# Optimization experiments

Measured on AMD Instinct MI355X. Metric: run time of the kernel, lower is better.

Reference implementation:

```python
import jax, jax.numpy as jnp
import numpy as np

B, N, D = 8, 1024, 512
H = 8
DH = D // H
EPS_DIST = 1e-8
EPS_LN = 1e-5


def _layer_norm(x, gamma, beta):
    mu = jnp.mean(x, axis=-1, keepdims=True)
    var = jnp.mean((x - mu) ** 2, axis=-1, keepdims=True)
    return (x - mu) * jax.lax.rsqrt(var + EPS_LN) * gamma + beta


def setup_inputs() -> dict:
    key = jax.random.key(0)
    ks = jax.random.split(key, 6)
    scale = 1.0 / np.sqrt(D)
    inp = {
        "x": jax.random.normal(ks[0], (B, N, D), dtype=jnp.float32),
        "Wq": jax.random.normal(ks[1], (D, D), dtype=jnp.float32) * scale,
        "Wk": jax.random.normal(ks[2], (D, D), dtype=jnp.float32) * scale,
        "Wv": jax.random.normal(ks[3], (D, D), dtype=jnp.float32) * scale,
        "Wo": jax.random.normal(ks[4], (D, D), dtype=jnp.float32) * scale,
        "bq": jnp.zeros((D,), jnp.float32),
        "bk": jnp.zeros((D,), jnp.float32),
        "bv": jnp.zeros((D,), jnp.float32),
        "bo": jnp.zeros((D,), jnp.float32),
        "ln1_g": jnp.ones((D,), jnp.float32),
        "ln1_b": jnp.zeros((D,), jnp.float32),
        "ln2_g": jnp.ones((D,), jnp.float32),
        "ln2_b": jnp.zeros((D,), jnp.float32),
    }
    return inp


def reference(x, Wq, bq, Wk, bk, Wv, bv, Wo, bo, ln1_g, ln1_b, ln2_g, ln2_b):
    residual = x
    h = _layer_norm(x, ln1_g, ln1_b)  # pre-norm

    def heads(t):
        # [B,N,D] -> [B,H,N,DH]
        return t.reshape(B, N, H, DH).transpose(0, 2, 1, 3)

    q = heads(h @ Wq + bq)
    k = heads(h @ Wk + bk)
    v = heads(h @ Wv + bv)

    # Euclidean pairwise distance via ||q||^2 + ||k||^2 - 2 q.k expansion
    q_sq = jnp.sum(q * q, axis=-1)[..., :, None]      # [B,H,N,1]
    k_sq = jnp.sum(k * k, axis=-1)[..., None, :]      # [B,H,1,N]
    qk = jnp.einsum("bhnd,bhmd->bhnm", q, k)          # [B,H,N,N]
    d2 = jnp.maximum(q_sq + k_sq - 2.0 * qk, 0.0)
    dist = jnp.sqrt(d2 + EPS_DIST)

    # distance -> attention score: smaller distance = higher attention
    attn = jax.nn.softmax(-dist, axis=-1)             # [B,H,N,N]

    out = jnp.einsum("bhnm,bhmd->bhnd", attn, v)      # [B,H,N,DH]
    out = out.transpose(0, 2, 1, 3).reshape(B, N, D)
    out = out @ Wo + bo

    y = residual + out
    y = _layer_norm(y, ln2_g, ln2_b)
    return y
```

## Files before the change

### kernel.cpp

```cpp
#include <hip/hip_runtime.h>
#include <math.h>

typedef __attribute__((ext_vector_type(8))) short short8;
typedef __attribute__((ext_vector_type(4))) float f32x4;

constexpr int B  = 8;
constexpr int N  = 1024;
constexpr int D  = 512;
constexpr int H  = 8;
constexpr int DH = 64;
constexpr int M_ROWS = 8192;
constexpr float EPS_DIST = 1e-8f;
constexpr float EPS_LN   = 1e-5f;

__device__ inline unsigned short bfbits(float f) {
    union { float f; unsigned u; } v; v.f = f;
    unsigned r = v.u + 0x7fffu + ((v.u >> 16) & 1u);
    return (unsigned short)(r >> 16);
}
__device__ inline float bf2f(unsigned short s) {
    union { unsigned u; float f; } v; v.u = ((unsigned)s) << 16; return v.f;
}

__device__ inline void async_ld16(unsigned short* lds, const unsigned short* g) {
    __builtin_amdgcn_global_load_lds(
        (const __attribute__((address_space(1))) unsigned int*)(g),
        (__attribute__((address_space(3))) unsigned int*)(lds),
        16, 0, 0);
}

__global__ __launch_bounds__(256) void wconv_kernel(const float* __restrict__ Wq,
                                                    const float* __restrict__ Wk,
                                                    const float* __restrict__ Wv,
                                                    const float* __restrict__ Wo,
                                                    unsigned short* __restrict__ WtAll) {
    int bx = blockIdx.x;
    int sub = bx >> 6;
    const float* W = sub == 0 ? Wq : sub == 1 ? Wk : sub == 2 ? Wv : Wo;
    unsigned short* Wt = WtAll + (size_t)sub * 262144;
    int t = (bx & 63) * 256 + threadIdx.x;
    int tn = t & 127, tk = t >> 7;
    int k = tk * 4, n = tn * 4;
    float4 r0 = *(const float4*)&W[(size_t)(k + 0) * 512 + n];
    float4 r1 = *(const float4*)&W[(size_t)(k + 1) * 512 + n];
    float4 r2 = *(const float4*)&W[(size_t)(k + 2) * 512 + n];
    float4 r3 = *(const float4*)&W[(size_t)(k + 3) * 512 + n];
    ushort4 c;
    c.x = bfbits(r0.x); c.y = bfbits(r1.x); c.z = bfbits(r2.x); c.w = bfbits(r3.x);
    *(ushort4*)&Wt[(size_t)(n + 0) * 512 + k] = c;
    c.x = bfbits(r0.y); c.y = bfbits(r1.y); c.z = bfbits(r2.y); c.w = bfbits(r3.y);
    *(ushort4*)&Wt[(size_t)(n + 1) * 512 + k] = c;
    c.x = bfbits(r0.z); c.y = bfbits(r1.z); c.z = bfbits(r2.z); c.w = bfbits(r3.z);
    *(ushort4*)&Wt[(size_t)(n + 2) * 512 + k] = c;
    c.x = bfbits(r0.w); c.y = bfbits(r1.w); c.z = bfbits(r2.w); c.w = bfbits(r3.w);
    *(ushort4*)&Wt[(size_t)(n + 3) * 512 + k] = c;
}

__device__ inline float block_sum256(float s, float* red) {
    for (int o = 32; o > 0; o >>= 1) s += __shfl_down(s, o, 64);
    int lane = threadIdx.x & 63, wid = threadIdx.x >> 6;
    if (lane == 0) red[wid] = s;
    __syncthreads();
    if (threadIdx.x == 0) red[4] = red[0] + red[1] + red[2] + red[3];
    __syncthreads();
    return red[4];
}

template <int OUT_BF16>
__global__ __launch_bounds__(256) void ln_kernel(const float* __restrict__ x,
                                                 const float* __restrict__ res,
                                                 const float* __restrict__ gamma,
                                                 const float* __restrict__ beta,
                                                 void* __restrict__ out) {
    __shared__ float red[8];
    const int row = blockIdx.x;
    const int t = threadIdx.x;
    const float* xr = x + (size_t)row * D;
    float v0 = xr[t], v1 = xr[t + 256];
    if (res) {
        const float* rr = res + (size_t)row * D;
        v0 += rr[t]; v1 += rr[t + 256];
    }
    float mu = block_sum256(v0 + v1, red) * (1.0f / D);
    float d0 = v0 - mu, d1 = v1 - mu;
    float var = block_sum256(d0 * d0 + d1 * d1, red) * (1.0f / D);
    float rstd = rsqrtf(var + EPS_LN);
    float o0 = d0 * rstd * gamma[t] + beta[t];
    float o1 = d1 * rstd * gamma[t + 256] + beta[t + 256];
    if (OUT_BF16) {
        ((unsigned short*)out)[(size_t)row * D + t]       = bfbits(o0);
        ((unsigned short*)out)[(size_t)row * D + t + 256] = bfbits(o1);
    } else {
        ((float*)out)[(size_t)row * D + t]       = o0;
        ((float*)out)[(size_t)row * D + t + 256] = o1;
    }
}

template <int MODE>
__global__ __launch_bounds__(256) void gemm128(const unsigned short* __restrict__ A,
                                               const unsigned short* __restrict__ Wt,
                                               const float* __restrict__ bias0,
                                               const float* __restrict__ bias1,
                                               const float* __restrict__ bias2,
                                               void* __restrict__ o0,
                                               unsigned short* __restrict__ Ko,
                                               unsigned short* __restrict__ Vo,
                                               float* __restrict__ sq0,
                                               float* __restrict__ sq1) {
    __shared__ unsigned short As[128 * 32];
    __shared__ unsigned short Bs[128 * 32];

    const int tid = threadIdx.x;
    const int lane = tid & 63, wv = tid >> 6;
    const int quad = lane >> 4, l15 = lane & 15;
    const int row0 = blockIdx.y * 128, col0 = blockIdx.x * 128;
    const int wm = (wv & 1) * 64, wn = (wv >> 1) * 64;

    f32x4 acc[4][4];
    #pragma unroll
    for (int i = 0; i < 4; ++i)
        #pragma unroll
        for (int j = 0; j < 4; ++j) acc[i][j] = (f32x4){0.f, 0.f, 0.f, 0.f};

    const unsigned short* Ag = A  + (size_t)row0 * 512;
    const unsigned short* Bg = Wt + (size_t)col0 * 512;

    for (int k0 = 0; k0 < 512; k0 += 32) {
        __syncthreads();
        #pragma unroll
        for (int c = 0; c < 2; ++c) {
            int fu = c * 2048 + tid * 8;
            int r = fu >> 5, ko = fu & 31;
            async_ld16(As + fu, Ag + (size_t)r * 512 + k0 + ko);
            async_ld16(Bs + fu, Bg + (size_t)r * 512 + k0 + ko);
        }
        __syncthreads();

        short8 af[4], bf[4];
        #pragma unroll
        for (int i = 0; i < 4; ++i)
            af[i] = *(const short8*)&As[(wm + i * 16 + l15) * 32 + quad * 8];
        #pragma unroll
        for (int j = 0; j < 4; ++j)
            bf[j] = *(const short8*)&Bs[(wn + j * 16 + l15) * 32 + quad * 8];
        #pragma unroll
        for (int i = 0; i < 4; ++i)
            #pragma unroll
            for (int j = 0; j < 4; ++j)
                acc[i][j] = __builtin_amdgcn_mfma_f32_16x16x32_bf16(af[i], bf[j], acc[i][j], 0, 0, 0);
    }

    if (MODE == 0) {
        float* C = (float*)o0;
        #pragma unroll
        for (int i = 0; i < 4; ++i)
            #pragma unroll
            for (int j = 0; j < 4; ++j) {
                int col = col0 + wn + j * 16 + l15;
                float bv = bias0[col];
                #pragma unroll
                for (int r = 0; r < 4; ++r) {
                    int row = row0 + wm + i * 16 + quad * 4 + r;
                    C[(size_t)row * 512 + col] = acc[i][j][r] + bv;
                }
            }
    } else {
        const int colg = col0 + wn;
        const int seg = colg >> 9;
        const int hh = (colg & 511) >> 6;
        const float* bias = seg == 0 ? bias0 : seg == 1 ? bias1 : bias2;

        if (seg < 2) {
            unsigned short* dst = seg == 0 ? (unsigned short*)o0 : Ko;
            float* sq = seg == 0 ? sq0 : sq1;
            #pragma unroll
            for (int i = 0; i < 4; ++i) {
                const int m0 = row0 + wm + i * 16 + quad * 4;
                float ss[4] = {0.f, 0.f, 0.f, 0.f};
                #pragma unroll
                for (int j = 0; j < 4; ++j) {
                    float bvj = bias[hh * 64 + j * 16 + l15];
                    #pragma unroll
                    for (int r = 0; r < 4; ++r) {
                        float v = acc[i][j][r] + bvj;
                        unsigned short ub = bfbits(v);
                        float vr = bf2f(ub);
                        ss[r] += vr * vr;
                        int m = m0 + r;
                        int b_ = m >> 10, n_ = m & 1023;
                        dst[((size_t)((b_ * 8 + hh) * 1024) + n_) * 64 + j * 16 + l15] = ub;
                    }
                }
                #pragma unroll
                for (int r = 0; r < 4; ++r) {
                    float s = ss[r];
                    s += __shfl_xor(s, 1, 64);
                    s += __shfl_xor(s, 2, 64);
                    s += __shfl_xor(s, 4, 64);
                    s += __shfl_xor(s, 8, 64);
                    if (l15 == 0) {
                        int m = m0 + r;
                        sq[(size_t)((m >> 10) * 8 + hh) * 1024 + (m & 1023)] = s;
                    }
                }
            }
        } else {
            #pragma unroll
            for (int i = 0; i < 4; ++i) {
                const int m0 = row0 + wm + i * 16 + quad * 4;
                const int b_ = m0 >> 10, n_ = m0 & 1023;
                #pragma unroll
                for (int j = 0; j < 4; ++j) {
                    float bvj = bias[hh * 64 + j * 16 + l15];
                    ushort4 pk;
                    pk.x = bfbits(acc[i][j][0] + bvj);
                    pk.y = bfbits(acc[i][j][1] + bvj);
                    pk.z = bfbits(acc[i][j][2] + bvj);
                    pk.w = bfbits(acc[i][j][3] + bvj);
                    *(ushort4*)&Vo[((size_t)((b_ * 8 + hh) * 64) + j * 16 + l15) * 1024 + n_] = pk;
                }
            }
        }
    }
}

__global__ __launch_bounds__(256) void attn_kernel(const unsigned short* __restrict__ Q,
                                                   const unsigned short* __restrict__ K,
                                                   const unsigned short* __restrict__ Vt,
                                                   const float* __restrict__ qsq,
                                                   const float* __restrict__ ksq,
                                                   unsigned short* __restrict__ O) {
    __shared__ unsigned short Ks[64][72];
    __shared__ unsigned short Vs[64][72];
    __shared__ unsigned short Ps[4][32][72];
    __shared__ float ksq_s[64];

    const int bh = blockIdx.y;
    const int q0 = blockIdx.x * 128;
    const int tid = threadIdx.x;
    const int lane = tid & 63, w = tid >> 6;
    const int quad = lane >> 4, l15 = lane & 15;
    const int b_ = bh >> 3, h_ = bh & 7;

    const unsigned short* Qb = Q  + (size_t)bh * N * DH;
    const unsigned short* Kb = K  + (size_t)bh * N * DH;
    const unsigned short* Vb = Vt + (size_t)bh * DH * N;

    short8 qf[2][2];
    #pragma unroll
    for (int i = 0; i < 2; ++i) {
        const unsigned short* qp = Qb + (size_t)(q0 + w * 32 + i * 16 + l15) * 64 + quad * 8;
        qf[i][0] = *(const short8*)qp;
        qf[i][1] = *(const short8*)(qp + 32);
    }
    float qe[2][4];
    #pragma unroll
    for (int i = 0; i < 2; ++i)
        #pragma unroll
        for (int r = 0; r < 4; ++r)
            qe[i][r] = qsq[bh * N + q0 + w * 32 + i * 16 + quad * 4 + r] + EPS_DIST;

    f32x4 oacc[2][4];
    #pragma unroll
    for (int i = 0; i < 2; ++i)
        #pragma unroll
        for (int dt = 0; dt < 4; ++dt) oacc[i][dt] = (f32x4){0.f, 0.f, 0.f, 0.f};
    float dpart[2][4] = {};

    for (int kt = 0; kt < 16; ++kt) {
        __syncthreads();
        {
            int rr = tid >> 2, c = (tid & 3) * 16;
            const unsigned short* kg = Kb + (size_t)(kt * 64 + rr) * 64 + c;
            *(uint4*)&Ks[rr][c]     = *(const uint4*)kg;
            *(uint4*)&Ks[rr][c + 8] = *(const uint4*)(kg + 8);
            const unsigned short* vg = Vb + (size_t)rr * N + kt * 64 + c;
            *(uint4*)&Vs[rr][c]     = *(const uint4*)vg;
            *(uint4*)&Vs[rr][c + 8] = *(const uint4*)(vg + 8);
        }
        if (tid < 64) ksq_s[tid] = ksq[bh * N + kt * 64 + tid];
        __syncthreads();

        #pragma unroll
        for (int kb = 0; kb < 4; ++kb) {
            short8 kf0 = *(const short8*)&Ks[kb * 16 + l15][quad * 8];
            short8 kf1 = *(const short8*)&Ks[kb * 16 + l15][32 + quad * 8];
            float ks2 = ksq_s[kb * 16 + l15];
            #pragma unroll
            for (int i = 0; i < 2; ++i) {
                f32x4 sa = (f32x4){0.f, 0.f, 0.f, 0.f};
                sa = __builtin_amdgcn_mfma_f32_16x16x32_bf16(qf[i][0], kf0, sa, 0, 0, 0);
                sa = __builtin_amdgcn_mfma_f32_16x16x32_bf16(qf[i][1], kf1, sa, 0, 0, 0);
                #pragma unroll
                for (int r = 0; r < 4; ++r) {
                    float d2 = fmaf(-2.0f, sa[r], qe[i][r] + ks2);
                    d2 = fmaxf(d2, EPS_DIST);
                    float p = __expf(-__builtin_amdgcn_sqrtf(d2));
                    dpart[i][r] += p;
                    Ps[w][i * 16 + quad * 4 + r][kb * 16 + l15] = bfbits(p);
                }
            }
        }

        short8 vf[4][2];
        #pragma unroll
        for (int dt = 0; dt < 4; ++dt)
            #pragma unroll
            for (int kc = 0; kc < 2; ++kc)
                vf[dt][kc] = *(const short8*)&Vs[dt * 16 + l15][kc * 32 + quad * 8];
        #pragma unroll
        for (int i = 0; i < 2; ++i)
            #pragma unroll
            for (int kc = 0; kc < 2; ++kc) {
                short8 pf = *(const short8*)&Ps[w][i * 16 + l15][kc * 32 + quad * 8];
                #pragma unroll
                for (int dt = 0; dt < 4; ++dt)
                    oacc[i][dt] = __builtin_amdgcn_mfma_f32_16x16x32_bf16(pf, vf[dt][kc], oacc[i][dt], 0, 0, 0);
            }
    }

    float rinv[2][4];
    #pragma unroll
    for (int i = 0; i < 2; ++i)
        #pragma unroll
        for (int r = 0; r < 4; ++r) {
            float s = dpart[i][r];
            s += __shfl_xor(s, 1, 64);
            s += __shfl_xor(s, 2, 64);
            s += __shfl_xor(s, 4, 64);
            s += __shfl_xor(s, 8, 64);
            rinv[i][r] = 1.0f / s;
        }

    #pragma unroll
    for (int i = 0; i < 2; ++i)
        #pragma unroll
        for (int dt = 0; dt < 4; ++dt)
            #pragma unroll
            for (int r = 0; r < 4; ++r) {
                int n_ = q0 + w * 32 + i * 16 + quad * 4 + r;
                O[((size_t)(b_ * N + n_) * D) + h_ * DH + dt * 16 + l15] =
                    bfbits(oacc[i][dt][r] * rinv[i][r]);
            }
}

extern "C" void kernel_launch(void* const* d_in, const int* in_sizes, int n_in,
                              void* d_out, int out_size, void* d_ws, size_t ws_size,
                              hipStream_t stream) {
    const float* x     = (const float*)d_in[0];
    const float* Wq    = (const float*)d_in[1];
    const float* Wk    = (const float*)d_in[2];
    const float* Wv    = (const float*)d_in[3];
    const float* Wo    = (const float*)d_in[4];
    const float* bq    = (const float*)d_in[5];
    const float* bk    = (const float*)d_in[6];
    const float* bv    = (const float*)d_in[7];
    const float* bo    = (const float*)d_in[8];
    const float* ln1_g = (const float*)d_in[9];
    const float* ln1_b = (const float*)d_in[10];
    const float* ln2_g = (const float*)d_in[11];
    const float* ln2_b = (const float*)d_in[12];
    float* out = (float*)d_out;

    unsigned short* WtAll = (unsigned short*)d_ws;
    unsigned short* h_bf  = WtAll + 4 * 262144;
    unsigned short* Qb    = h_bf + 4194304;
    unsigned short* Kb    = Qb + 4194304;
    unsigned short* Vtg   = Kb + 4194304;
    unsigned short* Ob    = Vtg + 4194304;
    float* Y0  = (float*)(Ob + 4194304);
    float* qsq = Y0 + 4194304;
    float* ksq = qsq + 65536;

    wconv_kernel<<<256, 256, 0, stream>>>(Wq, Wk, Wv, Wo, WtAll);

    ln_kernel<1><<<M_ROWS, 256, 0, stream>>>(x, nullptr, ln1_g, ln1_b, h_bf);

    gemm128<1><<<dim3(12, 64), 256, 0, stream>>>(h_bf, WtAll, bq, bk, bv,
                                                 Qb, Kb, Vtg, qsq, ksq);

    attn_kernel<<<dim3(8, 64), 256, 0, stream>>>(Qb, Kb, Vtg, qsq, ksq, Ob);

    gemm128<0><<<dim3(4, 64), 256, 0, stream>>>(Ob, WtAll + 3 * 262144, bo,
                                                nullptr, nullptr, Y0,
                                                nullptr, nullptr, nullptr, nullptr);

    ln_kernel<0><<<M_ROWS, 256, 0, stream>>>(Y0, x, ln2_g, ln2_b, out);
}
```

Baseline: 207.9 us.

## Double-buffer attention K/V tiles, LDS-transpose V stores, bf16 out-proj, smaller tiles

The attention kernel now double-buffers K, V and ksq tiles: the next tile is prefetched into registers while the current one is computed, which removes one barrier per iteration. The QKV GEMM stages the transposed V output through LDS so global writes are coalesced 16-byte stores. The output projection uses 64-row tiles for more blocks, writes bf16 instead of fp32, and the final layernorm reads bf16. Grids become 1D with bh-major ordering for locality. The bf16 intermediate before the residual add and layernorm adds rounding error.

```diff
diff --git a/kernel.cpp b/kernel.cpp
--- a/kernel.cpp
+++ b/kernel.cpp
@@ -66,8 +66,8 @@
     return red[4];
 }
 
-template <int OUT_BF16>
-__global__ __launch_bounds__(256) void ln_kernel(const float* __restrict__ x,
+template <int OUT_BF16, int IN_BF16>
+__global__ __launch_bounds__(256) void ln_kernel(const void* __restrict__ xv,
                                                  const float* __restrict__ res,
                                                  const float* __restrict__ gamma,
                                                  const float* __restrict__ beta,
@@ -75,8 +75,14 @@
     __shared__ float red[8];
     const int row = blockIdx.x;
     const int t = threadIdx.x;
-    const float* xr = x + (size_t)row * D;
-    float v0 = xr[t], v1 = xr[t + 256];
+    float v0, v1;
+    if (IN_BF16) {
+        const unsigned short* xr = (const unsigned short*)xv + (size_t)row * D;
+        v0 = bf2f(xr[t]); v1 = bf2f(xr[t + 256]);
+    } else {
+        const float* xr = (const float*)xv + (size_t)row * D;
+        v0 = xr[t]; v1 = xr[t + 256];
+    }
     if (res) {
         const float* rr = res + (size_t)row * D;
         v0 += rr[t]; v1 += rr[t + 256];
@@ -96,7 +102,7 @@
     }
 }
 
-template <int MODE>
+template <int MODE, int MT>
 __global__ __launch_bounds__(256) void gemm128(const unsigned short* __restrict__ A,
                                                const unsigned short* __restrict__ Wt,
                                                const float* __restrict__ bias0,
@@ -107,18 +113,24 @@
                                                unsigned short* __restrict__ Vo,
                                                float* __restrict__ sq0,
                                                float* __restrict__ sq1) {
-    __shared__ unsigned short As[128 * 32];
-    __shared__ unsigned short Bs[128 * 32];
-
+    constexpr int RB = M_ROWS / MT;
+    constexpr int NI = MT / 32;
+    constexpr int SMSZ = (MODE == 1) ? 18432 : (MT * 32 + 4096);
+    __shared__ unsigned short smem[SMSZ];
+    unsigned short* As = smem;
+    unsigned short* Bs = smem + MT * 32;
+
+    const int id = blockIdx.x;
+    const int by = id & (RB - 1), bx = id / RB;
     const int tid = threadIdx.x;
     const int lane = tid & 63, wv = tid >> 6;
     const int quad = lane >> 4, l15 = lane & 15;
-    const int row0 = blockIdx.y * 128, col0 = blockIdx.x * 128;
-    const int wm = (wv & 1) * 64, wn = (wv >> 1) * 64;
-
-    f32x4 acc[4][4];
-    #pragma unroll
-    for (int i = 0; i < 4; ++i)
+    const int row0 = by * MT, col0 = bx * 128;
+    const int wm = (wv & 1) * (MT / 2), wn = (wv >> 1) * 64;
+
+    f32x4 acc[NI][4];
+    #pragma unroll
+    for (int i = 0; i < NI; ++i)
         #pragma unroll
         for (int j = 0; j < 4; ++j) acc[i][j] = (f32x4){0.f, 0.f, 0.f, 0.f};
 
@@ -127,33 +139,38 @@
 
     for (int k0 = 0; k0 < 512; k0 += 32) {
         __syncthreads();
+        #pragma unroll
+        for (int c = 0; c < MT * 32 / 2048; ++c) {
+            int fu = c * 2048 + tid * 8;
+            int r = fu >> 5, ko = fu & 31;
+            async_ld16(As + fu, Ag + (size_t)r * 512 + k0 + ko);
+        }
         #pragma unroll
         for (int c = 0; c < 2; ++c) {
             int fu = c * 2048 + tid * 8;
             int r = fu >> 5, ko = fu & 31;
-            async_ld16(As + fu, Ag + (size_t)r * 512 + k0 + ko);
             async_ld16(Bs + fu, Bg + (size_t)r * 512 + k0 + ko);
         }
         __syncthreads();
 
-        short8 af[4], bf[4];
-        #pragma unroll
-        for (int i = 0; i < 4; ++i)
+        short8 af[NI], bf[4];
+        #pragma unroll
+        for (int i = 0; i < NI; ++i)
             af[i] = *(const short8*)&As[(wm + i * 16 + l15) * 32 + quad * 8];
         #pragma unroll
         for (int j = 0; j < 4; ++j)
             bf[j] = *(const short8*)&Bs[(wn + j * 16 + l15) * 32 + quad * 8];
         #pragma unroll
-        for (int i = 0; i < 4; ++i)
+        for (int i = 0; i < NI; ++i)
             #pragma unroll
             for (int j = 0; j < 4; ++j)
                 acc[i][j] = __builtin_amdgcn_mfma_f32_16x16x32_bf16(af[i], bf[j], acc[i][j], 0, 0, 0);
     }
 
     if (MODE == 0) {
-        float* C = (float*)o0;
-        #pragma unroll
-        for (int i = 0; i < 4; ++i)
+        unsigned short* C = (unsigned short*)o0;
+        #pragma unroll
+        for (int i = 0; i < NI; ++i)
             #pragma unroll
             for (int j = 0; j < 4; ++j) {
                 int col = col0 + wn + j * 16 + l15;
@@ -161,7 +178,7 @@
                 #pragma unroll
                 for (int r = 0; r < 4; ++r) {
                     int row = row0 + wm + i * 16 + quad * 4 + r;
-                    C[(size_t)row * 512 + col] = acc[i][j][r] + bv;
+                    C[(size_t)row * 512 + col] = bfbits(acc[i][j][r] + bv);
                 }
             }
     } else {
@@ -174,7 +191,7 @@
             unsigned short* dst = seg == 0 ? (unsigned short*)o0 : Ko;
             float* sq = seg == 0 ? sq0 : sq1;
             #pragma unroll
-            for (int i = 0; i < 4; ++i) {
+            for (int i = 0; i < NI; ++i) {
                 const int m0 = row0 + wm + i * 16 + quad * 4;
                 float ss[4] = {0.f, 0.f, 0.f, 0.f};
                 #pragma unroll
@@ -205,10 +222,10 @@
                 }
             }
         } else {
-            #pragma unroll
-            for (int i = 0; i < 4; ++i) {
-                const int m0 = row0 + wm + i * 16 + quad * 4;
-                const int b_ = m0 >> 10, n_ = m0 & 1023;
+            __syncthreads();
+            unsigned short* T = smem + wv * 4608;
+            #pragma unroll
+            for (int i = 0; i < NI; ++i)
                 #pragma unroll
                 for (int j = 0; j < 4; ++j) {
                     float bvj = bias[hh * 64 + j * 16 + l15];
@@ -217,8 +234,17 @@
                     pk.y = bfbits(acc[i][j][1] + bvj);
                     pk.z = bfbits(acc[i][j][2] + bvj);
                     pk.w = bfbits(acc[i][j][3] + bvj);
-                    *(ushort4*)&Vo[((size_t)((b_ * 8 + hh) * 64) + j * 16 + l15) * 1024 + n_] = pk;
+                    *(ushort4*)&T[(j * 16 + l15) * 72 + i * 16 + quad * 4] = pk;
                 }
+            const int b_ = (row0 + wm) >> 10;
+            const int nbase = (row0 + wm) & 1023;
+            unsigned short* Vg = Vo + ((size_t)((b_ * 8 + hh) * 64)) * 1024 + nbase;
+            #pragma unroll
+            for (int it = 0; it < 8; ++it) {
+                int dl = it * 8 + (lane >> 3);
+                int nl = (lane & 7) * 8;
+                uint4 v = *(const uint4*)&T[dl * 72 + nl];
+                *(uint4*)&Vg[(size_t)dl * 1024 + nl] = v;
             }
         }
     }
@@ -230,13 +256,14 @@
                                                    const float* __restrict__ qsq,
                                                    const float* __restrict__ ksq,
                                                    unsigned short* __restrict__ O) {
-    __shared__ unsigned short Ks[64][72];
-    __shared__ unsigned short Vs[64][72];
+    __shared__ unsigned short Ks[2][64][72];
+    __shared__ unsigned short Vs[2][64][72];
     __shared__ unsigned short Ps[4][32][72];
-    __shared__ float ksq_s[64];
-
-    const int bh = blockIdx.y;
-    const int q0 = blockIdx.x * 128;
+    __shared__ float ksq_s[2][64];
+
+    const int id = blockIdx.x;
+    const int bh = id & 63, qb = id >> 6;
+    const int q0 = qb * 128;
     const int tid = threadIdx.x;
     const int lane = tid & 63, w = tid >> 6;
     const int quad = lane >> 4, l15 = lane & 15;
@@ -267,25 +294,39 @@
         for (int dt = 0; dt < 4; ++dt) oacc[i][dt] = (f32x4){0.f, 0.f, 0.f, 0.f};
     float dpart[2][4] = {};
 
+    const int rr = tid >> 2, cc = (tid & 3) * 16;
+    uint4 kreg0, kreg1, vreg0, vreg1;
+    float ksreg = 0.f;
+
+    {
+        const unsigned short* kg = Kb + (size_t)rr * 64 + cc;
+        kreg0 = *(const uint4*)kg; kreg1 = *(const uint4*)(kg + 8);
+        const unsigned short* vg = Vb + (size_t)rr * N + cc;
+        vreg0 = *(const uint4*)vg; vreg1 = *(const uint4*)(vg + 8);
+        if (tid < 64) ksreg = ksq[bh * N + tid];
+    }
+    *(uint4*)&Ks[0][rr][cc]     = kreg0;
+    *(uint4*)&Ks[0][rr][cc + 8] = kreg1;
+    *(uint4*)&Vs[0][rr][cc]     = vreg0;
+    *(uint4*)&Vs[0][rr][cc + 8] = vreg1;
+    if (tid < 64) ksq_s[0][tid] = ksreg;
+    __syncthreads();
+
     for (int kt = 0; kt < 16; ++kt) {
-        __syncthreads();
-        {
-            int rr = tid >> 2, c = (tid & 3) * 16;
-            const unsigned short* kg = Kb + (size_t)(kt * 64 + rr) * 64 + c;
-            *(uint4*)&Ks[rr][c]     = *(const uint4*)kg;
-            *(uint4*)&Ks[rr][c + 8] = *(const uint4*)(kg + 8);
-            const unsigned short* vg = Vb + (size_t)rr * N + kt * 64 + c;
-            *(uint4*)&Vs[rr][c]     = *(const uint4*)vg;
-            *(uint4*)&Vs[rr][c + 8] = *(const uint4*)(vg + 8);
-        }
-        if (tid < 64) ksq_s[tid] = ksq[bh * N + kt * 64 + tid];
-        __syncthreads();
+        const int cur = kt & 1;
+        if (kt < 15) {
+            const unsigned short* kg = Kb + (size_t)((kt + 1) * 64 + rr) * 64 + cc;
+            kreg0 = *(const uint4*)kg; kreg1 = *(const uint4*)(kg + 8);
+            const unsigned short* vg = Vb + (size_t)rr * N + (kt + 1) * 64 + cc;
+            vreg0 = *(const uint4*)vg; vreg1 = *(const uint4*)(vg + 8);
+            if (tid < 64) ksreg = ksq[bh * N + (kt + 1) * 64 + tid];
+        }
 
         #pragma unroll
         for (int kb = 0; kb < 4; ++kb) {
-            short8 kf0 = *(const short8*)&Ks[kb * 16 + l15][quad * 8];
-            short8 kf1 = *(const short8*)&Ks[kb * 16 + l15][32 + quad * 8];
-            float ks2 = ksq_s[kb * 16 + l15];
+            short8 kf0 = *(const short8*)&Ks[cur][kb * 16 + l15][quad * 8];
+            short8 kf1 = *(const short8*)&Ks[cur][kb * 16 + l15][32 + quad * 8];
+            float ks2 = ksq_s[cur][kb * 16 + l15];
             #pragma unroll
             for (int i = 0; i < 2; ++i) {
                 f32x4 sa = (f32x4){0.f, 0.f, 0.f, 0.f};
@@ -307,7 +348,7 @@
         for (int dt = 0; dt < 4; ++dt)
             #pragma unroll
             for (int kc = 0; kc < 2; ++kc)
-                vf[dt][kc] = *(const short8*)&Vs[dt * 16 + l15][kc * 32 + quad * 8];
+                vf[dt][kc] = *(const short8*)&Vs[cur][dt * 16 + l15][kc * 32 + quad * 8];
         #pragma unroll
         for (int i = 0; i < 2; ++i)
             #pragma unroll
@@ -317,6 +358,15 @@
                 for (int dt = 0; dt < 4; ++dt)
                     oacc[i][dt] = __builtin_amdgcn_mfma_f32_16x16x32_bf16(pf, vf[dt][kc], oacc[i][dt], 0, 0, 0);
             }
+
+        if (kt < 15) {
+            *(uint4*)&Ks[cur ^ 1][rr][cc]     = kreg0;
+            *(uint4*)&Ks[cur ^ 1][rr][cc + 8] = kreg1;
+            *(uint4*)&Vs[cur ^ 1][rr][cc]     = vreg0;
+            *(uint4*)&Vs[cur ^ 1][rr][cc + 8] = vreg1;
+            if (tid < 64) ksq_s[cur ^ 1][tid] = ksreg;
+        }
+        __syncthreads();
     }
 
     float rinv[2][4];
@@ -368,22 +418,22 @@
     unsigned short* Kb    = Qb + 4194304;
     unsigned short* Vtg   = Kb + 4194304;
     unsigned short* Ob    = Vtg + 4194304;
-    float* Y0  = (float*)(Ob + 4194304);
-    float* qsq = Y0 + 4194304;
+    unsigned short* Y0    = Ob + 4194304;
+    float* qsq = (float*)(Y0 + 4194304);
     float* ksq = qsq + 65536;
 
     wconv_kernel<<<256, 256, 0, stream>>>(Wq, Wk, Wv, Wo, WtAll);
 
-    ln_kernel<1><<<M_ROWS, 256, 0, stream>>>(x, nullptr, ln1_g, ln1_b, h_bf);
-
-    gemm128<1><<<dim3(12, 64), 256, 0, stream>>>(h_bf, WtAll, bq, bk, bv,
-                                                 Qb, Kb, Vtg, qsq, ksq);
-
-    attn_kernel<<<dim3(8, 64), 256, 0, stream>>>(Qb, Kb, Vtg, qsq, ksq, Ob);
-
-    gemm128<0><<<dim3(4, 64), 256, 0, stream>>>(Ob, WtAll + 3 * 262144, bo,
-                                                nullptr, nullptr, Y0,
-                                                nullptr, nullptr, nullptr, nullptr);
-
-    ln_kernel<0><<<M_ROWS, 256, 0, stream>>>(Y0, x, ln2_g, ln2_b, out);
-}
+    ln_kernel<1, 0><<<M_ROWS, 256, 0, stream>>>(x, nullptr, ln1_g, ln1_b, h_bf);
+
+    gemm128<1, 128><<<768, 256, 0, stream>>>(h_bf, WtAll, bq, bk, bv,
+                                             Qb, Kb, Vtg, qsq, ksq);
+
+    attn_kernel<<<512, 256, 0, stream>>>(Qb, Kb, Vtg, qsq, ksq, Ob);
+
+    gemm128<0, 64><<<512, 256, 0, stream>>>(Ob, WtAll + 3 * 262144, bo,
+                                            nullptr, nullptr, Y0,
+                                            nullptr, nullptr, nullptr, nullptr);
+
+    ln_kernel<0, 1><<<M_ROWS, 256, 0, stream>>>(Y0, x, ln2_g, ln2_b, out);
+}
```

Result: faster. 188.7 us (-9.2%).
